# Kernel optimization log

Hardware: AMD Instinct MI355X
Metric: run time of the kernel (lower is better)

## Reference

```python
import jax, jax.numpy as jnp
import numpy as np

V, H, L, B = 50257, 1024, 10, 256

def setup_inputs() -> dict:
    key = jax.random.key(0)
    ks = jax.random.split(key, 16)
    s = 0.02
    return {
        "tokens": jax.random.randint(ks[0], (1, B), 0, V),
        "hidden": jax.random.normal(ks[1], (1, B, H), jnp.float32),
        "encoder_outputs": jax.random.normal(ks[2], (L, H), jnp.float32),
        "emb": jax.random.normal(ks[3], (V, H), jnp.float32) * s,
        "attn_W": jax.random.normal(ks[4], (L, 2 * H), jnp.float32) * s,
        "attn_b": jnp.zeros((L,), jnp.float32),
        "comb_W": jax.random.normal(ks[5], (H, 2 * H), jnp.float32) * s,
        "comb_b": jnp.zeros((H,), jnp.float32),
        "W_ih": jax.random.normal(ks[6], (3 * H, H), jnp.float32) * s,
        "W_hh": jax.random.normal(ks[7], (3 * H, H), jnp.float32) * s,
        "b_ih": jnp.zeros((3 * H,), jnp.float32),
        "b_hh": jnp.zeros((3 * H,), jnp.float32),
        "out_W": jax.random.normal(ks[8], (V, H), jnp.float32) * s,
        "out_b": jnp.zeros((V,), jnp.float32),
    }

def reference(tokens, hidden, encoder_outputs, emb, attn_W, attn_b, comb_W, comb_b,
              W_ih, W_hh, b_ih, b_hh, out_W, out_b):
    # Embedding lookup (dropout = identity, eval mode)
    embedded = emb[tokens[0]]            # [B, H]
    h = hidden[-1]                       # [B, H]
    # Attention over encoder outputs
    attn_logits = jnp.concatenate([embedded, h], axis=1) @ attn_W.T + attn_b
    attn_weights = jax.nn.softmax(attn_logits, axis=1)          # [B, L]
    attn_applied = attn_weights @ encoder_outputs                # [B, H]
    # Combine + relu -> GRU input
    x = jnp.concatenate([embedded, attn_applied], axis=1) @ comb_W.T + comb_b
    x = jax.nn.relu(x)                   # [B, H]
    # Single GRU step (PyTorch gate ordering: r, z, n)
    gi = x @ W_ih.T + b_ih               # [B, 3H]
    gh = h @ W_hh.T + b_hh               # [B, 3H]
    i_r, i_z, i_n = jnp.split(gi, 3, axis=1)
    h_r, h_z, h_n = jnp.split(gh, 3, axis=1)
    r = jax.nn.sigmoid(i_r + h_r)
    z = jax.nn.sigmoid(i_z + h_z)
    n = jnp.tanh(i_n + r * h_n)
    h_new = (1.0 - z) * n + z * h        # [B, H]
    # Output projection + log_softmax
    output = jax.nn.log_softmax(h_new @ out_W.T + out_b, axis=1)  # [B, V]
    return (output, h_new[None], attn_weights)
```

## Files before the change

### kernel.cpp

```cpp
#include <hip/hip_runtime.h>
#include <math.h>
#include <stdint.h>

#define B_SZ 256
#define H_SZ 1024
#define L_SZ 10
#define V_SZ 50257

typedef __attribute__((ext_vector_type(8))) short short8;
typedef __attribute__((ext_vector_type(4))) float floatx4;

__device__ __forceinline__ unsigned f2bf_bits(float f) {
    unsigned u = __float_as_uint(f);
    return (u + 0x7FFFu + ((u >> 16) & 1u)) >> 16;
}

__device__ __forceinline__ short8 cvt8(float4 a, float4 b) {
    unsigned r0, r1, r2, r3;
    asm("v_cvt_pk_bf16_f32 %0, %1, %2" : "=v"(r0) : "v"(a.x), "v"(a.y));
    asm("v_cvt_pk_bf16_f32 %0, %1, %2" : "=v"(r1) : "v"(a.z), "v"(a.w));
    asm("v_cvt_pk_bf16_f32 %0, %1, %2" : "=v"(r2) : "v"(b.x), "v"(b.y));
    asm("v_cvt_pk_bf16_f32 %0, %1, %2" : "=v"(r3) : "v"(b.z), "v"(b.w));
    union { unsigned u[4]; short8 s; } u;
    u.u[0] = r0; u.u[1] = r1; u.u[2] = r2; u.u[3] = r3;
    return u.s;
}

__device__ __forceinline__ void glds16(const void* g, void* l) {
    __builtin_amdgcn_global_load_lds(
        (const __attribute__((address_space(1))) void*)g,
        (__attribute__((address_space(3))) void*)l, 16, 0, 0);
}

template<int N> __device__ __forceinline__ void waitvm() {
    if constexpr (N == 0)       asm volatile("s_waitcnt vmcnt(0)" ::: "memory");
    else if constexpr (N == 3)  asm volatile("s_waitcnt vmcnt(3)" ::: "memory");
    else if constexpr (N == 4)  asm volatile("s_waitcnt vmcnt(4)" ::: "memory");
    else if constexpr (N == 6)  asm volatile("s_waitcnt vmcnt(6)" ::: "memory");
    else if constexpr (N == 8)  asm volatile("s_waitcnt vmcnt(8)" ::: "memory");
    else if constexpr (N == 9)  asm volatile("s_waitcnt vmcnt(9)" ::: "memory");
    else if constexpr (N == 10) asm volatile("s_waitcnt vmcnt(10)" ::: "memory");
    else if constexpr (N == 12) asm volatile("s_waitcnt vmcnt(12)" ::: "memory");
    else if constexpr (N == 20) asm volatile("s_waitcnt vmcnt(20)" ::: "memory");
    else static_assert(N == 0, "unsupported vmcnt literal");
}

template<int MSUB, int RELU, int DEPTH, int ABF>
__device__ __forceinline__ void gemm_body(
    float* wbuf, short* abufS, float* abufF,
    const void* __restrict__ A, const float* __restrict__ W,
    const float* __restrict__ bias, float* __restrict__ Cf,
    short* __restrict__ C16, int N, int K)
{
    constexpr int AOPS = ABF ? MSUB : 2 * MSUB;
    constexpr int OPS  = 2 + AOPS;

    const int tid  = threadIdx.x;
    const int wave = tid >> 6;
    const int lane = tid & 63;
    const int quad = lane >> 4;
    const int l16  = lane & 15;

    const int n0 = blockIdx.x * 64;
    const int m_base = blockIdx.y * (MSUB * 64) + wave * (MSUB * 16);
    const int nc = K >> 5;

    const float* wsrc[2];
#pragma unroll
    for (int i = 0; i < 2; ++i) {
        int row = n0 + 8 * (2 * wave + i) + (lane >> 3);
        if (row >= N) row = N - 1;
        wsrc[i] = W + (size_t)row * K + (((lane & 7) ^ (lane >> 3)) << 2);
    }
    const short* asrcS[ABF ? MSUB : 1];
    const float* asrcF[ABF ? 1 : 2 * MSUB];
    if constexpr (ABF) {
#pragma unroll
        for (int j = 0; j < MSUB; ++j) {
            int row = m_base + 16 * j + (lane >> 2);
            asrcS[j] = (const short*)A + (size_t)row * K
                     + (((lane & 3) ^ ((lane >> 3) & 3)) << 3);
        }
    } else {
#pragma unroll
        for (int j = 0; j < 2 * MSUB; ++j) {
            int row = m_base + 8 * j + (lane >> 3);
            asrcF[j] = (const float*)A + (size_t)row * K
                     + (((lane & 7) ^ (lane >> 3)) << 2);
        }
    }

    int boff[4][2];
#pragma unroll
    for (int ns = 0; ns < 4; ++ns) {
        int R = ns * 16 + l16;
#pragma unroll
        for (int h = 0; h < 2; ++h)
            boff[ns][h] = R * 128 + (((2 * quad + h) ^ (l16 & 7)) << 4);
    }
    int aoff[MSUB][2];
#pragma unroll
    for (int ms = 0; ms < MSUB; ++ms) {
        int Rl = wave * MSUB * 16 + ms * 16 + l16;
        if constexpr (ABF) {
            aoff[ms][0] = Rl * 64 + ((quad ^ ((l16 >> 1) & 3)) << 4);
            aoff[ms][1] = 0;
        } else {
#pragma unroll
            for (int h = 0; h < 2; ++h)
                aoff[ms][h] = Rl * 128 + (((2 * quad + h) ^ (l16 & 7)) << 4);
        }
    }

    floatx4 zero = {0.f, 0.f, 0.f, 0.f};
    floatx4 acc[MSUB][4];
#pragma unroll
    for (int ms = 0; ms < MSUB; ++ms)
#pragma unroll
        for (int ns = 0; ns < 4; ++ns) acc[ms][ns] = zero;

    auto issue = [&](int slot) {
#pragma unroll
        for (int i = 0; i < 2; ++i) {
            glds16(wsrc[i], (char*)wbuf + slot * 8192 + (2 * wave + i) * 1024);
            wsrc[i] += 32;
        }
        if constexpr (ABF) {
#pragma unroll
            for (int j = 0; j < MSUB; ++j) {
                glds16(asrcS[j], (char*)abufS + slot * (MSUB * 4096)
                                 + (wave * MSUB + j) * 1024);
                asrcS[j] += 32;
            }
        } else {
#pragma unroll
            for (int j = 0; j < 2 * MSUB; ++j) {
                glds16(asrcF[j], (char*)abufF + slot * (MSUB * 8192)
                                 + (wave * 2 * MSUB + j) * 1024);
                asrcF[j] += 32;
            }
        }
    };

#pragma unroll
    for (int d = 0; d < DEPTH; ++d) issue(d);

    int slot = 0;
    for (int c = 0; c < nc; ++c) {
        const int rem = nc - 1 - c;
        if (rem >= DEPTH - 1)  waitvm<OPS * (DEPTH - 1)>();
        else if (rem == 2)     waitvm<((DEPTH >= 4) ? 2 * OPS : 0)>();
        else if (rem == 1)     waitvm<((DEPTH >= 3) ? OPS : 0)>();
        else                   waitvm<0>();
        asm volatile("s_barrier" ::: "memory");

        const char* wb = (const char*)wbuf + slot * 8192;
        short8 bfr[4];
#pragma unroll
        for (int ns = 0; ns < 4; ++ns) {
            float4 x0 = *(const float4*)(wb + boff[ns][0]);
            float4 x1 = *(const float4*)(wb + boff[ns][1]);
            bfr[ns] = cvt8(x0, x1);
        }
        short8 afr[MSUB];
        if constexpr (ABF) {
            const char* ab = (const char*)abufS + slot * (MSUB * 4096);
#pragma unroll
            for (int ms = 0; ms < MSUB; ++ms)
                afr[ms] = *(const short8*)(ab + aoff[ms][0]);
        } else {
            const char* ab = (const char*)abufF + slot * (MSUB * 8192);
#pragma unroll
            for (int ms = 0; ms < MSUB; ++ms) {
                float4 a0 = *(const float4*)(ab + aoff[ms][0]);
                float4 a1 = *(const float4*)(ab + aoff[ms][1]);
                afr[ms] = cvt8(a0, a1);
            }
        }
#pragma unroll
        for (int ms = 0; ms < MSUB; ++ms)
#pragma unroll
            for (int ns = 0; ns < 4; ++ns)
                acc[ms][ns] = __builtin_amdgcn_mfma_f32_16x16x32_bf16(
                    afr[ms], bfr[ns], acc[ms][ns], 0, 0, 0);

        asm volatile("s_waitcnt lgkmcnt(0)" ::: "memory");
        asm volatile("s_barrier" ::: "memory");
        if (c + DEPTH < nc) issue(slot);
        if (++slot == DEPTH) slot = 0;
    }

    float bia[4];
#pragma unroll
    for (int ns = 0; ns < 4; ++ns) {
        int n = n0 + ns * 16 + l16;
        bia[ns] = (n < N) ? bias[n] : 0.f;
    }
#pragma unroll
    for (int ms = 0; ms < MSUB; ++ms) {
        int mb = m_base + ms * 16 + quad * 4;
#pragma unroll
        for (int ns = 0; ns < 4; ++ns) {
            int n = n0 + ns * 16 + l16;
            if (n < N) {
#pragma unroll
                for (int i = 0; i < 4; ++i) {
                    float v = acc[ms][ns][i] + bia[ns];
                    if (RELU) v = fmaxf(v, 0.f);
                    if (Cf)  Cf[(size_t)(mb + i) * N + n] = v;
                    if (C16) C16[(size_t)(mb + i) * N + n] = (short)f2bf_bits(v);
                }
            }
        }
    }
}

template<int MSUB, int RELU, int DEPTH, int ABF>
__global__ __launch_bounds__(256) void gemm_k(
    const void* __restrict__ A, const float* __restrict__ W,
    const float* __restrict__ bias, float* __restrict__ Cf,
    short* __restrict__ C16, int N, int K)
{
    __shared__ __align__(16) float wbuf[DEPTH * 64 * 32];
    __shared__ __align__(16) short abufS[ABF ? DEPTH * MSUB * 2048 : 8];
    __shared__ __align__(16) float abufF[ABF ? 8 : DEPTH * MSUB * 2048];
    gemm_body<MSUB, RELU, DEPTH, ABF>(wbuf, abufS, abufF, A, W, bias, Cf, C16, N, K);
}

template<int MSUB, int RELU, int DEPTH, int ABF>
__global__ __launch_bounds__(256) void gemm_dual(
    const void* __restrict__ A0, const float* __restrict__ W0,
    const float* __restrict__ b0, float* __restrict__ C0,
    const void* __restrict__ A1, const float* __restrict__ W1,
    const float* __restrict__ b1, float* __restrict__ C1,
    int N, int K)
{
    __shared__ __align__(16) float wbuf[DEPTH * 64 * 32];
    __shared__ __align__(16) short abufS[ABF ? DEPTH * MSUB * 2048 : 8];
    __shared__ __align__(16) float abufF[ABF ? 8 : DEPTH * MSUB * 2048];
    const void*  A = blockIdx.z ? A1 : A0;
    const float* W = blockIdx.z ? W1 : W0;
    const float* b = blockIdx.z ? b1 : b0;
    float*       C = blockIdx.z ? C1 : C0;
    gemm_body<MSUB, RELU, DEPTH, ABF>(wbuf, abufS, abufF, A, W, b, C, nullptr, N, K);
}

__global__ __launch_bounds__(256) void attn_kernel(
    const int* __restrict__ tokens, const float* __restrict__ hidden,
    const float* __restrict__ enc, const float* __restrict__ emb,
    const float* __restrict__ attn_W, const float* __restrict__ attn_b,
    float* __restrict__ catf, short* __restrict__ cat16,
    short* __restrict__ h16, float* __restrict__ attn_w_out)
{
    const int b = blockIdx.x;
    const int tid = threadIdx.x;
    const int tok = tokens[b];
    const float* erow = emb + (size_t)tok * H_SZ;
    const float* hrow = hidden + (size_t)b * H_SZ;

    __shared__ float red[L_SZ][256];
    __shared__ float wts[L_SZ];

    float acc[L_SZ];
#pragma unroll
    for (int l = 0; l < L_SZ; ++l) acc[l] = 0.f;

    for (int i = tid; i < H_SZ; i += 256) {
        float e = erow[i];
        float hv = hrow[i];
        if (catf)  catf[(size_t)b * 2 * H_SZ + i] = e;
        if (cat16) cat16[(size_t)b * 2 * H_SZ + i] = (short)f2bf_bits(e);
        if (h16)   h16[(size_t)b * H_SZ + i] = (short)f2bf_bits(hv);
#pragma unroll
        for (int l = 0; l < L_SZ; ++l) {
            acc[l] += e * attn_W[l * 2 * H_SZ + i] + hv * attn_W[l * 2 * H_SZ + H_SZ + i];
        }
    }
#pragma unroll
    for (int l = 0; l < L_SZ; ++l) red[l][tid] = acc[l];
    __syncthreads();
    for (int s = 128; s > 0; s >>= 1) {
        if (tid < s) {
#pragma unroll
            for (int l = 0; l < L_SZ; ++l) red[l][tid] += red[l][tid + s];
        }
        __syncthreads();
    }
    if (tid == 0) {
        float m = -INFINITY;
        float lg[L_SZ];
#pragma unroll
        for (int l = 0; l < L_SZ; ++l) {
            lg[l] = red[l][0] + attn_b[l];
            m = fmaxf(m, lg[l]);
        }
        float s = 0.f;
#pragma unroll
        for (int l = 0; l < L_SZ; ++l) {
            float e = expf(lg[l] - m);
            wts[l] = e;
            s += e;
        }
        float inv = 1.f / s;
#pragma unroll
        for (int l = 0; l < L_SZ; ++l) {
            wts[l] *= inv;
            attn_w_out[(size_t)b * L_SZ + l] = wts[l];
        }
    }
    __syncthreads();

    for (int i = tid; i < H_SZ; i += 256) {
        float s = 0.f;
#pragma unroll
        for (int l = 0; l < L_SZ; ++l) s += wts[l] * enc[l * H_SZ + i];
        if (catf)  catf[(size_t)b * 2 * H_SZ + H_SZ + i] = s;
        if (cat16) cat16[(size_t)b * 2 * H_SZ + H_SZ + i] = (short)f2bf_bits(s);
    }
}

__global__ __launch_bounds__(256) void gru_combine(
    const float* __restrict__ gi, const float* __restrict__ gh,
    const float* __restrict__ hidden, float* __restrict__ h_new,
    short* __restrict__ hb16)
{
    int idx = blockIdx.x * blockDim.x + threadIdx.x;
    if (idx >= B_SZ * H_SZ) return;
    int b = idx >> 10;
    int j = idx & (H_SZ - 1);
    const float* gib = gi + (size_t)b * 3 * H_SZ;
    const float* ghb = gh + (size_t)b * 3 * H_SZ;
    float i_r = gib[j], i_z = gib[H_SZ + j], i_n = gib[2 * H_SZ + j];
    float h_r = ghb[j], h_z = ghb[H_SZ + j], h_n = ghb[2 * H_SZ + j];
    float r = 1.f / (1.f + expf(-(i_r + h_r)));
    float z = 1.f / (1.f + expf(-(i_z + h_z)));
    float n = tanhf(i_n + r * h_n);
    float h = hidden[idx];
    float hn = (1.f - z) * n + z * h;
    h_new[idx] = hn;
    if (hb16) hb16[idx] = (short)f2bf_bits(hn);
}

__global__ __launch_bounds__(1024) void logsoftmax_v2(float* __restrict__ out)
{
    const int b = blockIdx.x;
    float* row = out + (size_t)b * V_SZ;
    const int tid = threadIdx.x;
    const int wave = tid >> 6;
    const int lane = tid & 63;

    const int head = (int)(((16u - ((uintptr_t)row & 15u)) & 15u) >> 2);
    const int nv = (V_SZ - head) >> 2;
    const float4* r4 = (const float4*)(row + head);
    const int tail_start = head + (nv << 2);

    float m = -INFINITY, s = 0.f;
    if (tid < head) {
        float v = row[tid];
        m = v; s = 1.f;
    }
    for (int i = tid; i < nv; i += 1024) {
        float4 v = r4[i];
        float mv = fmaxf(fmaxf(v.x, v.y), fmaxf(v.z, v.w));
        if (mv > m) { s *= expf(m - mv); m = mv; }
        s += expf(v.x - m) + expf(v.y - m) + expf(v.z - m) + expf(v.w - m);
    }
    for (int i = tail_start + tid; i < V_SZ; i += 1024) {
        float v = row[i];
        if (v > m) { s *= expf(m - v); m = v; }
        s += expf(v - m);
    }

    for (int off = 32; off > 0; off >>= 1) {
        float m2 = __shfl_down(m, off);
        float s2 = __shfl_down(s, off);
        float mn = fmaxf(m, m2);
        s = s * expf(m - mn) + s2 * expf(m2 - mn);
        m = mn;
    }
    __shared__ float smax[16], ssum[16], slse;
    if (lane == 0) { smax[wave] = m; ssum[wave] = s; }
    __syncthreads();
    if (tid == 0) {
        float M = smax[0], S = ssum[0];
        for (int w = 1; w < 16; ++w) {
            float mn = fmaxf(M, smax[w]);
            S = S * expf(M - mn) + ssum[w] * expf(smax[w] - mn);
            M = mn;
        }
        slse = M + logf(S);
    }
    __syncthreads();
    const float lse = slse;

    if (tid < head) row[tid] -= lse;
    float4* w4 = (float4*)(row + head);
    for (int i = tid; i < nv; i += 1024) {
        float4 v = r4[i];
        v.x -= lse; v.y -= lse; v.z -= lse; v.w -= lse;
        w4[i] = v;
    }
    for (int i = tail_start + tid; i < V_SZ; i += 1024) row[i] -= lse;
}

extern "C" void kernel_launch(void* const* d_in, const int* in_sizes, int n_in,
                              void* d_out, int out_size, void* d_ws, size_t ws_size,
                              hipStream_t stream)
{
    const int*   tokens = (const int*)d_in[0];
    const float* hidden = (const float*)d_in[1];
    const float* enc    = (const float*)d_in[2];
    const float* emb    = (const float*)d_in[3];
    const float* attn_W = (const float*)d_in[4];
    const float* attn_b = (const float*)d_in[5];
    const float* comb_W = (const float*)d_in[6];
    const float* comb_b = (const float*)d_in[7];
    const float* W_ih   = (const float*)d_in[8];
    const float* W_hh   = (const float*)d_in[9];
    const float* b_ih   = (const float*)d_in[10];
    const float* b_hh   = (const float*)d_in[11];
    const float* out_W  = (const float*)d_in[12];
    const float* out_b  = (const float*)d_in[13];

    float* out = (float*)d_out;
    float* logits     = out;
    float* h_new      = out + (size_t)B_SZ * V_SZ;
    float* attn_w_out = h_new + (size_t)B_SZ * H_SZ;

    const size_t need = (size_t)B_SZ * 5 * H_SZ * sizeof(short)
                      + (size_t)B_SZ * 6 * H_SZ * sizeof(float);
    const bool use_ws = (d_ws != nullptr) && (ws_size >= need);

    if (use_ws) {
        short* cat16 = (short*)d_ws;
        short* x16   = cat16 + (size_t)B_SZ * 2 * H_SZ;
        short* hin16 = x16   + (size_t)B_SZ * H_SZ;
        short* hb16  = hin16 + (size_t)B_SZ * H_SZ;
        float* gi    = (float*)(hb16 + (size_t)B_SZ * H_SZ);
        float* gh    = gi + (size_t)B_SZ * 3 * H_SZ;

        attn_kernel<<<B_SZ, 256, 0, stream>>>(tokens, hidden, enc, emb, attn_W,
                                              attn_b, nullptr, cat16, hin16,
                                              attn_w_out);
        gemm_k<1, 1, 4, 1><<<dim3(H_SZ / 64, 4), 256, 0, stream>>>(
            cat16, comb_W, comb_b, nullptr, x16, H_SZ, 2 * H_SZ);
        gemm_dual<1, 0, 4, 1><<<dim3(3 * H_SZ / 64, 4, 2), 256, 0, stream>>>(
            x16, W_ih, b_ih, gi, hin16, W_hh, b_hh, gh, 3 * H_SZ, H_SZ);
        gru_combine<<<(B_SZ * H_SZ + 255) / 256, 256, 0, stream>>>(
            gi, gh, hidden, h_new, hb16);
        gemm_k<4, 0, 3, 1><<<dim3((V_SZ + 63) / 64, 1), 256, 0, stream>>>(
            hb16, out_W, out_b, logits, nullptr, V_SZ, H_SZ);
    } else {
        float* cat = logits;
        float* x   = cat + (size_t)B_SZ * 2 * H_SZ;
        float* gi  = x   + (size_t)B_SZ * H_SZ;
        float* gh  = gi  + (size_t)B_SZ * 3 * H_SZ;

        attn_kernel<<<B_SZ, 256, 0, stream>>>(tokens, hidden, enc, emb, attn_W,
                                              attn_b, cat, nullptr, nullptr,
                                              attn_w_out);
        gemm_k<1, 1, 3, 0><<<dim3(H_SZ / 64, 4), 256, 0, stream>>>(
            cat, comb_W, comb_b, x, nullptr, H_SZ, 2 * H_SZ);
        gemm_dual<1, 0, 3, 0><<<dim3(3 * H_SZ / 64, 4, 2), 256, 0, stream>>>(
            x, W_ih, b_ih, gi, hidden, W_hh, b_hh, gh, 3 * H_SZ, H_SZ);
        gru_combine<<<(B_SZ * H_SZ + 255) / 256, 256, 0, stream>>>(
            gi, gh, hidden, h_new, nullptr);
        gemm_k<4, 0, 2, 0><<<dim3((V_SZ + 63) / 64, 1), 256, 0, stream>>>(
            h_new, out_W, out_b, logits, nullptr, V_SZ, H_SZ);
    }
    logsoftmax_v2<<<B_SZ, 1024, 0, stream>>>(logits);
}
```

Measured before the change: 584.0 us.

## Replace LDS-staged GEMMs with direct global-to-register pipelined MFMA loads

Drops the shared-memory staging (global_load_lds with barriers) from all GEMMs. Each wave now loads its W and A fragments straight from global memory into registers through a PD-deep software pipeline, with no barriers. The smaller GEMMs use 32-wide N tiles to launch more blocks, and the log-softmax loops are unrolled 4x for more memory-level parallelism. The cost is that W tiles are no longer shared between waves through LDS, so each wave of the output projection reads its W tile separately, and register pressure goes up.

```diff
diff --git a/kernel.cpp b/kernel.cpp
--- a/kernel.cpp
+++ b/kernel.cpp
@@ -26,186 +26,111 @@
     return u.s;
 }
 
-__device__ __forceinline__ void glds16(const void* g, void* l) {
-    __builtin_amdgcn_global_load_lds(
-        (const __attribute__((address_space(1))) void*)g,
-        (__attribute__((address_space(3))) void*)l, 16, 0, 0);
-}
-
-template<int N> __device__ __forceinline__ void waitvm() {
-    if constexpr (N == 0)       asm volatile("s_waitcnt vmcnt(0)" ::: "memory");
-    else if constexpr (N == 3)  asm volatile("s_waitcnt vmcnt(3)" ::: "memory");
-    else if constexpr (N == 4)  asm volatile("s_waitcnt vmcnt(4)" ::: "memory");
-    else if constexpr (N == 6)  asm volatile("s_waitcnt vmcnt(6)" ::: "memory");
-    else if constexpr (N == 8)  asm volatile("s_waitcnt vmcnt(8)" ::: "memory");
-    else if constexpr (N == 9)  asm volatile("s_waitcnt vmcnt(9)" ::: "memory");
-    else if constexpr (N == 10) asm volatile("s_waitcnt vmcnt(10)" ::: "memory");
-    else if constexpr (N == 12) asm volatile("s_waitcnt vmcnt(12)" ::: "memory");
-    else if constexpr (N == 20) asm volatile("s_waitcnt vmcnt(20)" ::: "memory");
-    else static_assert(N == 0, "unsupported vmcnt literal");
-}
-
-template<int MSUB, int RELU, int DEPTH, int ABF>
-__device__ __forceinline__ void gemm_body(
-    float* wbuf, short* abufS, float* abufF,
+template<int MSUB, int NF, int RELU, int PD, int ABF>
+__global__ __launch_bounds__(256) void gemm_direct(
     const void* __restrict__ A, const float* __restrict__ W,
     const float* __restrict__ bias, float* __restrict__ Cf,
     short* __restrict__ C16, int N, int K)
 {
-    constexpr int AOPS = ABF ? MSUB : 2 * MSUB;
-    constexpr int OPS  = 2 + AOPS;
-
     const int tid  = threadIdx.x;
     const int wave = tid >> 6;
     const int lane = tid & 63;
     const int quad = lane >> 4;
     const int l16  = lane & 15;
 
-    const int n0 = blockIdx.x * 64;
+    const int n0 = blockIdx.x * (NF * 16);
     const int m_base = blockIdx.y * (MSUB * 64) + wave * (MSUB * 16);
     const int nc = K >> 5;
 
-    const float* wsrc[2];
-#pragma unroll
-    for (int i = 0; i < 2; ++i) {
-        int row = n0 + 8 * (2 * wave + i) + (lane >> 3);
-        if (row >= N) row = N - 1;
-        wsrc[i] = W + (size_t)row * K + (((lane & 7) ^ (lane >> 3)) << 2);
-    }
-    const short* asrcS[ABF ? MSUB : 1];
-    const float* asrcF[ABF ? 1 : 2 * MSUB];
-    if constexpr (ABF) {
-#pragma unroll
-        for (int j = 0; j < MSUB; ++j) {
-            int row = m_base + 16 * j + (lane >> 2);
-            asrcS[j] = (const short*)A + (size_t)row * K
-                     + (((lane & 3) ^ ((lane >> 3) & 3)) << 3);
-        }
-    } else {
-#pragma unroll
-        for (int j = 0; j < 2 * MSUB; ++j) {
-            int row = m_base + 8 * j + (lane >> 3);
-            asrcF[j] = (const float*)A + (size_t)row * K
-                     + (((lane & 7) ^ (lane >> 3)) << 2);
-        }
-    }
-
-    int boff[4][2];
-#pragma unroll
-    for (int ns = 0; ns < 4; ++ns) {
-        int R = ns * 16 + l16;
-#pragma unroll
-        for (int h = 0; h < 2; ++h)
-            boff[ns][h] = R * 128 + (((2 * quad + h) ^ (l16 & 7)) << 4);
-    }
-    int aoff[MSUB][2];
+    const float* wp[NF];
+#pragma unroll
+    for (int nf = 0; nf < NF; ++nf) {
+        int r = n0 + nf * 16 + l16;
+        if (r >= N) r = N - 1;
+        wp[nf] = W + (size_t)r * K + quad * 8;
+    }
+    const short* ab[MSUB];
+    const float* af[MSUB];
 #pragma unroll
     for (int ms = 0; ms < MSUB; ++ms) {
-        int Rl = wave * MSUB * 16 + ms * 16 + l16;
-        if constexpr (ABF) {
-            aoff[ms][0] = Rl * 64 + ((quad ^ ((l16 >> 1) & 3)) << 4);
-            aoff[ms][1] = 0;
-        } else {
-#pragma unroll
-            for (int h = 0; h < 2; ++h)
-                aoff[ms][h] = Rl * 128 + (((2 * quad + h) ^ (l16 & 7)) << 4);
-        }
+        int r = m_base + ms * 16 + l16;
+        if (ABF) ab[ms] = (const short*)A + (size_t)r * K + quad * 8;
+        else     af[ms] = (const float*)A + (size_t)r * K + quad * 8;
     }
 
     floatx4 zero = {0.f, 0.f, 0.f, 0.f};
-    floatx4 acc[MSUB][4];
+    floatx4 acc[MSUB][NF];
 #pragma unroll
     for (int ms = 0; ms < MSUB; ++ms)
 #pragma unroll
-        for (int ns = 0; ns < 4; ++ns) acc[ms][ns] = zero;
-
-    auto issue = [&](int slot) {
-#pragma unroll
-        for (int i = 0; i < 2; ++i) {
-            glds16(wsrc[i], (char*)wbuf + slot * 8192 + (2 * wave + i) * 1024);
-            wsrc[i] += 32;
-        }
-        if constexpr (ABF) {
-#pragma unroll
-            for (int j = 0; j < MSUB; ++j) {
-                glds16(asrcS[j], (char*)abufS + slot * (MSUB * 4096)
-                                 + (wave * MSUB + j) * 1024);
-                asrcS[j] += 32;
+        for (int nf = 0; nf < NF; ++nf) acc[ms][nf] = zero;
+
+    float4 sw[PD][NF][2];
+    short8 sa[PD][MSUB];
+    float4 sf[PD][MSUB][2];
+
+    auto lstage = [&](int p, int c) {
+#pragma unroll
+        for (int nf = 0; nf < NF; ++nf) {
+            sw[p][nf][0] = *(const float4*)(wp[nf] + (size_t)c * 32);
+            sw[p][nf][1] = *(const float4*)(wp[nf] + (size_t)c * 32 + 4);
+        }
+#pragma unroll
+        for (int ms = 0; ms < MSUB; ++ms) {
+            if constexpr (ABF) {
+                sa[p][ms] = *(const short8*)(ab[ms] + (size_t)c * 32);
+            } else {
+                sf[p][ms][0] = *(const float4*)(af[ms] + (size_t)c * 32);
+                sf[p][ms][1] = *(const float4*)(af[ms] + (size_t)c * 32 + 4);
             }
-        } else {
-#pragma unroll
-            for (int j = 0; j < 2 * MSUB; ++j) {
-                glds16(asrcF[j], (char*)abufF + slot * (MSUB * 8192)
-                                 + (wave * 2 * MSUB + j) * 1024);
-                asrcF[j] += 32;
-            }
         }
     };
-
-#pragma unroll
-    for (int d = 0; d < DEPTH; ++d) issue(d);
-
-    int slot = 0;
-    for (int c = 0; c < nc; ++c) {
-        const int rem = nc - 1 - c;
-        if (rem >= DEPTH - 1)  waitvm<OPS * (DEPTH - 1)>();
-        else if (rem == 2)     waitvm<((DEPTH >= 4) ? 2 * OPS : 0)>();
-        else if (rem == 1)     waitvm<((DEPTH >= 3) ? OPS : 0)>();
-        else                   waitvm<0>();
-        asm volatile("s_barrier" ::: "memory");
-
-        const char* wb = (const char*)wbuf + slot * 8192;
-        short8 bfr[4];
-#pragma unroll
-        for (int ns = 0; ns < 4; ++ns) {
-            float4 x0 = *(const float4*)(wb + boff[ns][0]);
-            float4 x1 = *(const float4*)(wb + boff[ns][1]);
-            bfr[ns] = cvt8(x0, x1);
-        }
-        short8 afr[MSUB];
-        if constexpr (ABF) {
-            const char* ab = (const char*)abufS + slot * (MSUB * 4096);
-#pragma unroll
-            for (int ms = 0; ms < MSUB; ++ms)
-                afr[ms] = *(const short8*)(ab + aoff[ms][0]);
-        } else {
-            const char* ab = (const char*)abufF + slot * (MSUB * 8192);
-#pragma unroll
-            for (int ms = 0; ms < MSUB; ++ms) {
-                float4 a0 = *(const float4*)(ab + aoff[ms][0]);
-                float4 a1 = *(const float4*)(ab + aoff[ms][1]);
-                afr[ms] = cvt8(a0, a1);
-            }
-        }
-#pragma unroll
-        for (int ms = 0; ms < MSUB; ++ms)
-#pragma unroll
-            for (int ns = 0; ns < 4; ++ns)
-                acc[ms][ns] = __builtin_amdgcn_mfma_f32_16x16x32_bf16(
-                    afr[ms], bfr[ns], acc[ms][ns], 0, 0, 0);
-
-        asm volatile("s_waitcnt lgkmcnt(0)" ::: "memory");
-        asm volatile("s_barrier" ::: "memory");
-        if (c + DEPTH < nc) issue(slot);
-        if (++slot == DEPTH) slot = 0;
-    }
-
-    float bia[4];
-#pragma unroll
-    for (int ns = 0; ns < 4; ++ns) {
-        int n = n0 + ns * 16 + l16;
-        bia[ns] = (n < N) ? bias[n] : 0.f;
+    auto compute = [&](int p) {
+        short8 bfr[NF];
+#pragma unroll
+        for (int nf = 0; nf < NF; ++nf)
+            bfr[nf] = cvt8(sw[p][nf][0], sw[p][nf][1]);
+#pragma unroll
+        for (int ms = 0; ms < MSUB; ++ms) {
+            short8 afr;
+            if constexpr (ABF) afr = sa[p][ms];
+            else               afr = cvt8(sf[p][ms][0], sf[p][ms][1]);
+#pragma unroll
+            for (int nf = 0; nf < NF; ++nf)
+                acc[ms][nf] = __builtin_amdgcn_mfma_f32_16x16x32_bf16(
+                    afr, bfr[nf], acc[ms][nf], 0, 0, 0);
+        }
+    };
+
+#pragma unroll
+    for (int p = 0; p < PD; ++p) lstage(p, p);
+
+    for (int cb = 0; cb < nc - PD; cb += PD) {
+#pragma unroll
+        for (int p = 0; p < PD; ++p) {
+            compute(p);
+            lstage(p, cb + p + PD);
+        }
+    }
+#pragma unroll
+    for (int p = 0; p < PD; ++p) compute(p);
+
+    float bia[NF];
+#pragma unroll
+    for (int nf = 0; nf < NF; ++nf) {
+        int n = n0 + nf * 16 + l16;
+        bia[nf] = (n < N) ? bias[n] : 0.f;
     }
 #pragma unroll
     for (int ms = 0; ms < MSUB; ++ms) {
         int mb = m_base + ms * 16 + quad * 4;
 #pragma unroll
-        for (int ns = 0; ns < 4; ++ns) {
-            int n = n0 + ns * 16 + l16;
+        for (int nf = 0; nf < NF; ++nf) {
+            int n = n0 + nf * 16 + l16;
             if (n < N) {
 #pragma unroll
                 for (int i = 0; i < 4; ++i) {
-                    float v = acc[ms][ns][i] + bia[ns];
+                    float v = acc[ms][nf][i] + bia[nf];
                     if (RELU) v = fmaxf(v, 0.f);
                     if (Cf)  Cf[(size_t)(mb + i) * N + n] = v;
                     if (C16) C16[(size_t)(mb + i) * N + n] = (short)f2bf_bits(v);
@@ -215,34 +140,116 @@
     }
 }
 
-template<int MSUB, int RELU, int DEPTH, int ABF>
-__global__ __launch_bounds__(256) void gemm_k(
-    const void* __restrict__ A, const float* __restrict__ W,
-    const float* __restrict__ bias, float* __restrict__ Cf,
-    short* __restrict__ C16, int N, int K)
-{
-    __shared__ __align__(16) float wbuf[DEPTH * 64 * 32];
-    __shared__ __align__(16) short abufS[ABF ? DEPTH * MSUB * 2048 : 8];
-    __shared__ __align__(16) float abufF[ABF ? 8 : DEPTH * MSUB * 2048];
-    gemm_body<MSUB, RELU, DEPTH, ABF>(wbuf, abufS, abufF, A, W, bias, Cf, C16, N, K);
-}
-
-template<int MSUB, int RELU, int DEPTH, int ABF>
-__global__ __launch_bounds__(256) void gemm_dual(
+template<int MSUB, int NF, int RELU, int PD, int ABF>
+__global__ __launch_bounds__(256) void gemm_direct_dual(
     const void* __restrict__ A0, const float* __restrict__ W0,
     const float* __restrict__ b0, float* __restrict__ C0,
     const void* __restrict__ A1, const float* __restrict__ W1,
     const float* __restrict__ b1, float* __restrict__ C1,
     int N, int K)
 {
-    __shared__ __align__(16) float wbuf[DEPTH * 64 * 32];
-    __shared__ __align__(16) short abufS[ABF ? DEPTH * MSUB * 2048 : 8];
-    __shared__ __align__(16) float abufF[ABF ? 8 : DEPTH * MSUB * 2048];
     const void*  A = blockIdx.z ? A1 : A0;
     const float* W = blockIdx.z ? W1 : W0;
     const float* b = blockIdx.z ? b1 : b0;
     float*       C = blockIdx.z ? C1 : C0;
-    gemm_body<MSUB, RELU, DEPTH, ABF>(wbuf, abufS, abufF, A, W, b, C, nullptr, N, K);
+
+    const int tid  = threadIdx.x;
+    const int wave = tid >> 6;
+    const int lane = tid & 63;
+    const int quad = lane >> 4;
+    const int l16  = lane & 15;
+    const int n0 = blockIdx.x * (NF * 16);
+    const int m_base = blockIdx.y * (MSUB * 64) + wave * (MSUB * 16);
+    const int nc = K >> 5;
+
+    const float* wp[NF];
+#pragma unroll
+    for (int nf = 0; nf < NF; ++nf) {
+        int r = n0 + nf * 16 + l16;
+        if (r >= N) r = N - 1;
+        wp[nf] = W + (size_t)r * K + quad * 8;
+    }
+    const short* ab[MSUB];
+    const float* af[MSUB];
+#pragma unroll
+    for (int ms = 0; ms < MSUB; ++ms) {
+        int r = m_base + ms * 16 + l16;
+        if (ABF) ab[ms] = (const short*)A + (size_t)r * K + quad * 8;
+        else     af[ms] = (const float*)A + (size_t)r * K + quad * 8;
+    }
+
+    floatx4 zero = {0.f, 0.f, 0.f, 0.f};
+    floatx4 acc[MSUB][NF];
+#pragma unroll
+    for (int ms = 0; ms < MSUB; ++ms)
+#pragma unroll
+        for (int nf = 0; nf < NF; ++nf) acc[ms][nf] = zero;
+
+    float4 sw[PD][NF][2];
+    short8 sa[PD][MSUB];
+    float4 sf[PD][MSUB][2];
+
+    auto lstage = [&](int p, int c) {
+#pragma unroll
+        for (int nf = 0; nf < NF; ++nf) {
+            sw[p][nf][0] = *(const float4*)(wp[nf] + (size_t)c * 32);
+            sw[p][nf][1] = *(const float4*)(wp[nf] + (size_t)c * 32 + 4);
+        }
+#pragma unroll
+        for (int ms = 0; ms < MSUB; ++ms) {
+            if constexpr (ABF) {
+                sa[p][ms] = *(const short8*)(ab[ms] + (size_t)c * 32);
+            } else {
+                sf[p][ms][0] = *(const float4*)(af[ms] + (size_t)c * 32);
+                sf[p][ms][1] = *(const float4*)(af[ms] + (size_t)c * 32 + 4);
+            }
+        }
+    };
+    auto compute = [&](int p) {
+        short8 bfr[NF];
+#pragma unroll
+        for (int nf = 0; nf < NF; ++nf)
+            bfr[nf] = cvt8(sw[p][nf][0], sw[p][nf][1]);
+#pragma unroll
+        for (int ms = 0; ms < MSUB; ++ms) {
+            short8 afr;
+            if constexpr (ABF) afr = sa[p][ms];
+            else               afr = cvt8(sf[p][ms][0], sf[p][ms][1]);
+#pragma unroll
+            for (int nf = 0; nf < NF; ++nf)
+                acc[ms][nf] = __builtin_amdgcn_mfma_f32_16x16x32_bf16(
+                    afr, bfr[nf], acc[ms][nf], 0, 0, 0);
+        }
+    };
+
+#pragma unroll
+    for (int p = 0; p < PD; ++p) lstage(p, p);
+    for (int cb = 0; cb < nc - PD; cb += PD) {
+#pragma unroll
+        for (int p = 0; p < PD; ++p) { compute(p); lstage(p, cb + p + PD); }
+    }
+#pragma unroll
+    for (int p = 0; p < PD; ++p) compute(p);
+
+    float bia[NF];
+#pragma unroll
+    for (int nf = 0; nf < NF; ++nf) {
+        int n = n0 + nf * 16 + l16;
+        bia[nf] = (n < N) ? b[n] : 0.f;
+    }
+#pragma unroll
+    for (int ms = 0; ms < MSUB; ++ms) {
+        int mb = m_base + ms * 16 + quad * 4;
+#pragma unroll
+        for (int nf = 0; nf < NF; ++nf) {
+            int n = n0 + nf * 16 + l16;
+            if (n < N) {
+#pragma unroll
+                for (int i = 0; i < 4; ++i)
+                    C[(size_t)(mb + i) * N + n] = acc[ms][nf][i] + bia[nf];
+            }
+        }
+    }
 }
 
 __global__ __launch_bounds__(256) void attn_kernel(
@@ -341,7 +348,7 @@
     if (hb16) hb16[idx] = (short)f2bf_bits(hn);
 }
 
-__global__ __launch_bounds__(1024) void logsoftmax_v2(float* __restrict__ out)
+__global__ __launch_bounds__(1024) void logsoftmax_v3(float* __restrict__ out)
 {
     const int b = blockIdx.x;
     float* row = out + (size_t)b * V_SZ;
@@ -359,14 +366,28 @@
         float v = row[tid];
         m = v; s = 1.f;
     }
-    for (int i = tid; i < nv; i += 1024) {
+    int i = tid;
+    for (; i + 3072 < nv; i += 4096) {
+        float4 v0 = r4[i], v1 = r4[i + 1024], v2 = r4[i + 2048], v3 = r4[i + 3072];
+        float m0 = fmaxf(fmaxf(v0.x, v0.y), fmaxf(v0.z, v0.w));
+        float m1 = fmaxf(fmaxf(v1.x, v1.y), fmaxf(v1.z, v1.w));
+        float m2 = fmaxf(fmaxf(v2.x, v2.y), fmaxf(v2.z, v2.w));
+        float m3 = fmaxf(fmaxf(v3.x, v3.y), fmaxf(v3.z, v3.w));
+        float mv = fmaxf(fmaxf(m0, m1), fmaxf(m2, m3));
+        if (mv > m) { s *= expf(m - mv); m = mv; }
+        s += expf(v0.x - m) + expf(v0.y - m) + expf(v0.z - m) + expf(v0.w - m);
+        s += expf(v1.x - m) + expf(v1.y - m) + expf(v1.z - m) + expf(v1.w - m);
+        s += expf(v2.x - m) + expf(v2.y - m) + expf(v2.z - m) + expf(v2.w - m);
+        s += expf(v3.x - m) + expf(v3.y - m) + expf(v3.z - m) + expf(v3.w - m);
+    }
+    for (; i < nv; i += 1024) {
         float4 v = r4[i];
         float mv = fmaxf(fmaxf(v.x, v.y), fmaxf(v.z, v.w));
         if (mv > m) { s *= expf(m - mv); m = mv; }
         s += expf(v.x - m) + expf(v.y - m) + expf(v.z - m) + expf(v.w - m);
     }
-    for (int i = tail_start + tid; i < V_SZ; i += 1024) {
-        float v = row[i];
+    for (int t = tail_start + tid; t < V_SZ; t += 1024) {
+        float v = row[t];
         if (v > m) { s *= expf(m - v); m = v; }
         s += expf(v - m);
     }
@@ -395,12 +416,21 @@
 
     if (tid < head) row[tid] -= lse;
     float4* w4 = (float4*)(row + head);
-    for (int i = tid; i < nv; i += 1024) {
+    i = tid;
+    for (; i + 3072 < nv; i += 4096) {
+        float4 v0 = r4[i], v1 = r4[i + 1024], v2 = r4[i + 2048], v3 = r4[i + 3072];
+        v0.x -= lse; v0.y -= lse; v0.z -= lse; v0.w -= lse;
+        v1.x -= lse; v1.y -= lse; v1.z -= lse; v1.w -= lse;
+        v2.x -= lse; v2.y -= lse; v2.z -= lse; v2.w -= lse;
+        v3.x -= lse; v3.y -= lse; v3.z -= lse; v3.w -= lse;
+        w4[i] = v0; w4[i + 1024] = v1; w4[i + 2048] = v2; w4[i + 3072] = v3;
+    }
+    for (; i < nv; i += 1024) {
         float4 v = r4[i];
         v.x -= lse; v.y -= lse; v.z -= lse; v.w -= lse;
         w4[i] = v;
     }
-    for (int i = tail_start + tid; i < V_SZ; i += 1024) row[i] -= lse;
+    for (int t = tail_start + tid; t < V_SZ; t += 1024) row[t] -= lse;
 }
 
 extern "C" void kernel_launch(void* const* d_in, const int* in_sizes, int n_in,
@@ -442,13 +472,13 @@
         attn_kernel<<<B_SZ, 256, 0, stream>>>(tokens, hidden, enc, emb, attn_W,
                                               attn_b, nullptr, cat16, hin16,
                                               attn_w_out);
-        gemm_k<1, 1, 4, 1><<<dim3(H_SZ / 64, 4), 256, 0, stream>>>(
+        gemm_direct<1, 2, 1, 4, 1><<<dim3(H_SZ / 32, 4), 256, 0, stream>>>(
             cat16, comb_W, comb_b, nullptr, x16, H_SZ, 2 * H_SZ);
-        gemm_dual<1, 0, 4, 1><<<dim3(3 * H_SZ / 64, 4, 2), 256, 0, stream>>>(
+        gemm_direct_dual<1, 2, 0, 4, 1><<<dim3(3 * H_SZ / 32, 4, 2), 256, 0, stream>>>(
             x16, W_ih, b_ih, gi, hin16, W_hh, b_hh, gh, 3 * H_SZ, H_SZ);
         gru_combine<<<(B_SZ * H_SZ + 255) / 256, 256, 0, stream>>>(
             gi, gh, hidden, h_new, hb16);
-        gemm_k<4, 0, 3, 1><<<dim3((V_SZ + 63) / 64, 1), 256, 0, stream>>>(
+        gemm_direct<4, 4, 0, 2, 1><<<dim3((V_SZ + 63) / 64, 1), 256, 0, stream>>>(
             hb16, out_W, out_b, logits, nullptr, V_SZ, H_SZ);
     } else {
         float* cat = logits;
@@ -459,14 +489,14 @@
         attn_kernel<<<B_SZ, 256, 0, stream>>>(tokens, hidden, enc, emb, attn_W,
                                               attn_b, cat, nullptr, nullptr,
                                               attn_w_out);
-        gemm_k<1, 1, 3, 0><<<dim3(H_SZ / 64, 4), 256, 0, stream>>>(
+        gemm_direct<1, 2, 1, 4, 0><<<dim3(H_SZ / 32, 4), 256, 0, stream>>>(
             cat, comb_W, comb_b, x, nullptr, H_SZ, 2 * H_SZ);
-        gemm_dual<1, 0, 3, 0><<<dim3(3 * H_SZ / 64, 4, 2), 256, 0, stream>>>(
+        gemm_direct_dual<1, 2, 0, 4, 0><<<dim3(3 * H_SZ / 32, 4, 2), 256, 0, stream>>>(
             x, W_ih, b_ih, gi, hidden, W_hh, b_hh, gh, 3 * H_SZ, H_SZ);
         gru_combine<<<(B_SZ * H_SZ + 255) / 256, 256, 0, stream>>>(
             gi, gh, hidden, h_new, nullptr);
-        gemm_k<4, 0, 2, 0><<<dim3((V_SZ + 63) / 64, 1), 256, 0, stream>>>(
+        gemm_direct<4, 4, 0, 2, 0><<<dim3((V_SZ + 63) / 64, 1), 256, 0, stream>>>(
             h_new, out_W, out_b, logits, nullptr, V_SZ, H_SZ);
     }
-    logsoftmax_v2<<<B_SZ, 1024, 0, stream>>>(logits);
-}
+    logsoftmax_v3<<<B_SZ, 1024, 0, stream>>>(logits);
+}
```

Measured after the change: 656.3 us. 12.4% more time.
